# Performance work log

Hardware: AMD Instinct MI355X
Metric: run time of the kernel (lower is better)

The kernel has to match this reference:

```python
import jax, jax.numpy as jnp
import numpy as np

HEADS = 4
ATTN_DIM = 32
SCALE = ATTN_DIM ** -0.5
EPS = 1e-12  # F.normalize eps


def rmsnorm_chan(x, g):
    # x: (b, c, h, w); RMSNorm over channel dim: F.normalize(x, dim=1) * g * sqrt(c)
    c = x.shape[1]
    n = jnp.sqrt(jnp.sum(x * x, axis=1, keepdims=True))
    return x / jnp.maximum(n, EPS) * g[None, :, None, None] * jnp.sqrt(jnp.asarray(c, x.dtype))


def setup_inputs() -> dict:
    key = jax.random.key(0)
    ks = jax.random.split(key, 4)
    b, c, h, w = 16, 256, 64, 64
    hidden = HEADS * ATTN_DIM  # 128
    x = jax.random.normal(ks[0], (b, c, h, w), dtype=jnp.float32)
    norm_g = jnp.ones((c,), jnp.float32)
    w_qkv = jax.random.normal(ks[1], (3 * hidden, c), dtype=jnp.float32) * 0.02
    mem_kv = jax.random.normal(ks[2], (2, HEADS, ATTN_DIM, 4), dtype=jnp.float32)
    w_out = jax.random.normal(ks[3], (c, hidden), dtype=jnp.float32) * 0.02
    b_out = jnp.zeros((c,), jnp.float32)
    out_norm_g = jnp.ones((c,), jnp.float32)
    return {"x": x, "norm_g": norm_g, "w_qkv": w_qkv, "mem_kv": mem_kv,
            "w_out": w_out, "b_out": b_out, "out_norm_g": out_norm_g}


def reference(x, norm_g, w_qkv, mem_kv, w_out, b_out, out_norm_g):
    b, c, h, w = x.shape
    n = h * w
    xn = rmsnorm_chan(x, norm_g).reshape(b, c, n)  # pre-norm, flatten spatial
    # 1x1 conv (no bias) == channel matmul: (b, 3*hidden, n)
    qkv = jnp.einsum('oc,bcn->bon', w_qkv, xn)
    q, k, v = jnp.split(qkv, 3, axis=1)
    # (b, heads, d, n)
    q = q.reshape(b, HEADS, ATTN_DIM, n)
    k = k.reshape(b, HEADS, ATTN_DIM, n)
    v = v.reshape(b, HEADS, ATTN_DIM, n)
    # prepend memory kv (broadcast over batch): (b, heads, d, num_mem + n)
    mk = jnp.broadcast_to(mem_kv[0][None], (b, HEADS, ATTN_DIM, mem_kv.shape[-1]))
    mv = jnp.broadcast_to(mem_kv[1][None], (b, HEADS, ATTN_DIM, mem_kv.shape[-1]))
    k = jnp.concatenate([mk, k], axis=-1)
    v = jnp.concatenate([mv, v], axis=-1)
    q = jax.nn.softmax(q, axis=-2) * SCALE  # softmax over feature dim d
    k = jax.nn.softmax(k, axis=-1)          # softmax over token dim n
    context = jnp.einsum('bhdn,bhen->bhde', k, v)   # small d x e per head
    out = jnp.einsum('bhde,bhdn->bhen', context, q)  # (b, heads, e, n)
    out = out.reshape(b, HEADS * ATTN_DIM, h, w)
    # 1x1 conv with bias, then RMSNorm
    out = jnp.einsum('oc,bchw->bohw', w_out, out) + b_out[None, :, None, None]
    return rmsnorm_chan(out, out_norm_g)
```

## Files before the change

kernel.cpp:

```cpp
#include <hip/hip_runtime.h>
#include <hip/hip_bf16.h>

typedef __hip_bfloat16 bf16;
typedef __attribute__((ext_vector_type(8))) short bf16x8;
typedef __attribute__((ext_vector_type(4))) float floatx4;

#define NB 16
#define NC 256
#define NPIX 4096
#define NHID 128
#define NH 4
#define ND 32
#define NMEM 4
#define QSCALE 0.17677669529663687f

__launch_bounds__(256)
__global__ void kW(const float* __restrict__ wqkv, const float* __restrict__ g,
                   bf16* __restrict__ wgpack, float* __restrict__ zbase){
  const int u = blockIdx.x*256 + threadIdx.x;
  for (int z = u; z < 65536 + 2048; z += 48*256) zbase[z] = 0.f;
  const int s = u / 1536;
  const int r = u - s*1536;
  const int tile = r >> 6, l = r & 63;
  const int row = tile*16 + (l & 15);
  const int kb  = s*32 + (l >> 4)*8;
  const float* wp = wqkv + (size_t)row*NC + kb;
  floatx4 w0 = *(const floatx4*)wp;
  floatx4 w1 = *(const floatx4*)(wp + 4);
  floatx4 g0 = *(const floatx4*)(g + kb);
  floatx4 g1 = *(const floatx4*)(g + kb + 4);
  alignas(16) bf16 tmp[8];
  #pragma unroll
  for (int i = 0; i < 4; ++i){
    tmp[i]   = __float2bfloat16(w0[i]*g0[i]);
    tmp[4+i] = __float2bfloat16(w1[i]*g1[i]);
  }
  *(uint4*)(wgpack + (size_t)u*8) = *(const uint4*)tmp;
}

__launch_bounds__(256)
__global__ void kA(const float* __restrict__ x, const bf16* __restrict__ wgpack,
                   float* __restrict__ dout,
                   float* __restrict__ ctxu, float* __restrict__ zacc){
  __shared__ char smem alignas(16) [21632];
  bf16 (*Pb)[40] = (bf16(*)[40])smem;
  bf16 (*Vb)[40] = (bf16(*)[40])(smem + 10240);
  float* ssqL = (float*)(smem + 20480);
  float* sL   = (float*)(smem + 21504);
  const int t = threadIdx.x;
  const int bx = blockIdx.x, b = blockIdx.y;
  const int pb32 = bx * 32;
  const int pb64 = (bx >> 1) * 64, hi = bx & 1;
  const int wv = t >> 6, lane = t & 63, m = lane & 15, q4 = lane >> 4;
  const int px_st = t & 31, cg_st = t >> 5;
  const float* xb = x + (size_t)b*NC*NPIX;
  float ssq = 0.f;
  float xr[2][4];
  bf16x8 af[2][6];

  auto xissue = [&](int c, float* dst){
    const float* xp = xb + (size_t)(c*32 + cg_st*4)*NPIX + pb32 + px_st;
    #pragma unroll
    for (int j = 0; j < 4; ++j) dst[j] = xp[(size_t)j*NPIX];
  };
  auto xwrite = [&](int c, const float* v){
    alignas(8) bf16 tmp[4];
    #pragma unroll
    for (int j = 0; j < 4; ++j){
      ssq += v[j]*v[j];
      tmp[j] = __float2bfloat16(v[j]);
    }
    bf16 (*Xb)[40] = (bf16(*)[40])(smem + (c&1)*2560);
    *(uint2*)&Xb[px_st][cg_st*4] = *(const uint2*)tmp;
  };
  auto wload = [&](int c, int rt)->bf16x8 {
    return *(const bf16x8*)(wgpack + ((size_t)(c*24 + wv*6 + rt)*64 + lane)*8);
  };

  xissue(0, xr[0]);
  #pragma unroll
  for (int rt = 0; rt < 6; ++rt) af[0][rt] = wload(0, rt);
  xissue(1, xr[1]);
  xwrite(0, xr[0]);
  __syncthreads();

  floatx4 acc[6][2] = {};
  #pragma unroll
  for (int s = 0; s < 8; ++s){
    const int buf = s & 1;
    bf16 (*Xb)[40] = (bf16(*)[40])(smem + buf*2560);
    bf16x8 bfr[2];
    #pragma unroll
    for (int pt = 0; pt < 2; ++pt)
      bfr[pt] = *(const bf16x8*)&Xb[pt*16 + m][q4*8];
    if (s < 7){
      #pragma unroll
      for (int rt = 0; rt < 6; ++rt) af[(s+1)&1][rt] = wload(s + 1, rt);
    }
    if (s < 6) xissue(s + 2, xr[buf]);
    #pragma unroll
    for (int rt = 0; rt < 6; ++rt)
      #pragma unroll
      for (int pt = 0; pt < 2; ++pt)
        acc[rt][pt] = __builtin_amdgcn_mfma_f32_16x16x32_bf16(af[buf][rt], bfr[pt], acc[rt][pt], 0, 0, 0);
    if (s < 7) xwrite(s + 1, xr[buf ^ 1]);
    __syncthreads();
  }
  ssqL[cg_st*32 + px_st] = ssq;
  __syncthreads();
  if (t < 32){
    float tot = 0.f;
    #pragma unroll
    for (int i = 0; i < 8; ++i) tot += ssqL[i*32 + t];
    sL[t] = 16.0f / fmaxf(sqrtf(tot), 1e-12f);
  }
  __syncthreads();
  float sv[2];
  #pragma unroll
  for (int pt = 0; pt < 2; ++pt) sv[pt] = sL[pt*16 + m];
  #pragma unroll
  for (int pr = 0; pr < 3; ++pr){
    const int ra = 2*pr, rb = 2*pr + 1;
    const int row0 = wv*96 + pr*32;
    const int type = row0 >> 7;
    if (type == 0){
      const int slice = row0 >> 5;
      const int j0 = (q4 & 1)*4;
      #pragma unroll
      for (int pt = 0; pt < 2; ++pt){
        float va[4], vb[4];
        float mx = -1e30f;
        #pragma unroll
        for (int r = 0; r < 4; ++r){
          va[r] = acc[ra][pt][r]*sv[pt];
          vb[r] = acc[rb][pt][r]*sv[pt];
          mx = fmaxf(mx, fmaxf(va[r], vb[r]));
        }
        mx = fmaxf(mx, __shfl_xor(mx, 16, 64));
        mx = fmaxf(mx, __shfl_xor(mx, 32, 64));
        float se = 0.f;
        #pragma unroll
        for (int r = 0; r < 4; ++r){
          va[r] = __expf(va[r] - mx); vb[r] = __expf(vb[r] - mx);
          se += va[r] + vb[r];
        }
        se += __shfl_xor(se, 16, 64);
        se += __shfl_xor(se, 32, 64);
        const float inv = QSCALE / se;
        alignas(8) bf16 pka[4], pkb[4];
        #pragma unroll
        for (int r = 0; r < 4; ++r){
          pka[r] = __float2bfloat16(va[r]*inv);
          pkb[r] = __float2bfloat16(vb[r]*inv);
        }
        const int ca = (slice*4 + (hi*2 + pt))*4 + (q4 >> 1);
        const int cb = ca + 2;
        bf16* pa = (bf16*)(dout + (size_t)(b*NC + ca)*NPIX + pb64) + m*8 + j0;
        bf16* pv = (bf16*)(dout + (size_t)(b*NC + cb)*NPIX + pb64) + m*8 + j0;
        *(uint2*)pa = *(const uint2*)pka;
        *(uint2*)pv = *(const uint2*)pkb;
      }
    } else if (type == 1){
      const int d0 = row0 - 128;
      float za[4] = {}, zb[4] = {};
      #pragma unroll
      for (int pt = 0; pt < 2; ++pt){
        #pragma unroll
        for (int r = 0; r < 4; ++r){
          float pa = __expf(acc[ra][pt][r]*sv[pt]);
          float pv = __expf(acc[rb][pt][r]*sv[pt]);
          za[r] += pa; zb[r] += pv;
          Pb[d0      + q4*4 + r][pt*16 + m] = __float2bfloat16(pa);
          Pb[d0 + 16 + q4*4 + r][pt*16 + m] = __float2bfloat16(pv);
        }
      }
      #pragma unroll
      for (int r = 0; r < 4; ++r){
        #pragma unroll
        for (int o = 1; o < 16; o <<= 1){
          za[r] += __shfl_xor(za[r], o, 64);
          zb[r] += __shfl_xor(zb[r], o, 64);
        }
      }
      if (m == 0){
        #pragma unroll
        for (int r = 0; r < 4; ++r){
          atomicAdd(&zacc[b*NHID + d0      + q4*4 + r], za[r]);
          atomicAdd(&zacc[b*NHID + d0 + 16 + q4*4 + r], zb[r]);
        }
      }
    } else {
      const int v0 = row0 - 256;
      #pragma unroll
      for (int pt = 0; pt < 2; ++pt)
        #pragma unroll
        for (int r = 0; r < 4; ++r){
          Vb[v0      + q4*4 + r][pt*16 + m] = __float2bfloat16(acc[ra][pt][r]*sv[pt]);
          Vb[v0 + 16 + q4*4 + r][pt*16 + m] = __float2bfloat16(acc[rb][pt][r]*sv[pt]);
        }
    }
  }
  __syncthreads();
  floatx4 cx[2][2] = {};
  {
    bf16x8 af2[2], bf2[2];
    #pragma unroll
    for (int dt = 0; dt < 2; ++dt) af2[dt] = *(const bf16x8*)&Pb[wv*32 + dt*16 + m][q4*8];
    #pragma unroll
    for (int et = 0; et < 2; ++et) bf2[et] = *(const bf16x8*)&Vb[wv*32 + et*16 + m][q4*8];
    #pragma unroll
    for (int dt = 0; dt < 2; ++dt)
      #pragma unroll
      for (int et = 0; et < 2; ++et)
        cx[dt][et] = __builtin_amdgcn_mfma_f32_16x16x32_bf16(af2[dt], bf2[et], cx[dt][et], 0, 0, 0);
  }
  float* cb2 = ctxu + (size_t)(b*NH + wv)*ND*ND;
  #pragma unroll
  for (int dt = 0; dt < 2; ++dt)
    #pragma unroll
    for (int et = 0; et < 2; ++et)
      #pragma unroll
      for (int r = 0; r < 4; ++r)
        atomicAdd(&cb2[(dt*16 + q4*4 + r)*ND + et*16 + m], cx[dt][et][r]);
}

__launch_bounds__(256)
__global__ void k4_weff(const float* __restrict__ ctxu, const float* __restrict__ zacc,
                        const float* __restrict__ memkv, const float* __restrict__ wout,
                        bf16* __restrict__ wpack){
  __shared__ float ctxL[4][32][32];
  __shared__ float woutL[64][129];
  const int t = threadIdx.x;
  const int o0 = blockIdx.x * 64, b = blockIdx.y;
  {
    const float* ws = wout + (size_t)o0*NHID;
    #pragma unroll
    for (int i = 0; i < 32; ++i){
      const int idx = i*256 + t;
      woutL[idx >> 7][idx & 127] = ws[idx];
    }
  }
  if (t < 128){
    const int h = t >> 5;
    const float* mk = memkv + t*NMEM;
    float me[4]; float z = zacc[b*NHID + t];
    #pragma unroll
    for (int j = 0; j < 4; ++j){ me[j] = __expf(mk[j]); z += me[j]; }
    const float invz = 1.0f / z;
    const float* cp = ctxu + (size_t)(b*NH*ND + t)*ND;
    const float* mv = memkv + (size_t)(NHID + h*ND)*NMEM;
    #pragma unroll
    for (int e = 0; e < ND; ++e){
      float ce = cp[e];
      #pragma unroll
      for (int j = 0; j < 4; ++j) ce += me[j]*mv[e*NMEM + j];
      ctxL[h][t & 31][e] = ce * invz;
    }
  }
  __syncthreads();
  const int ol = t & 63, g = t >> 6;
  float out[32] = {};
  #pragma unroll
  for (int e = 0; e < 32; ++e){
    const float we = woutL[ol][g*32 + e];
    #pragma unroll
    for (int d = 0; d < 32; ++d) out[d] += ctxL[g][d][e] * we;
  }
  const int o = o0 + ol, tile = o >> 4, m16 = o & 15;
  #pragma unroll
  for (int q4k = 0; q4k < 4; ++q4k){
    alignas(16) bf16 tmp[8];
    #pragma unroll
    for (int j = 0; j < 8; ++j) tmp[j] = __float2bfloat16(out[q4k*8 + j]);
    *(uint4*)(wpack + ((size_t)((b*4 + g)*16 + tile)*64 + q4k*16 + m16)*8) = *(const uint4*)tmp;
  }
}

__launch_bounds__(256)
__global__ void k5_out(float* dout, const bf16* __restrict__ wpack,
                       const float* __restrict__ bout, const float* __restrict__ gout){
  __shared__ float red[256];
  __shared__ float nf[64];
  const int t = threadIdx.x;
  const int pb = blockIdx.x * 64, b = blockIdx.y;
  const int wv = t >> 6, lane = t & 63, m = lane & 15, q4 = lane >> 4;
  bf16x8 wf[2][4], qf[2][4];
  auto loadw = [&](int s, bf16x8* dst){
    #pragma unroll
    for (int rt = 0; rt < 4; ++rt)
      dst[rt] = *(const bf16x8*)(wpack + ((size_t)((b*4 + s)*16 + wv*4 + rt)*64 + lane)*8);
  };
  auto loadq = [&](int s, bf16x8* dst){
    #pragma unroll
    for (int pt = 0; pt < 4; ++pt)
      dst[pt] = *(const bf16x8*)((const char*)(dout + (size_t)(b*NC + (s*4 + pt)*4 + q4)*NPIX + pb) + m*16);
  };
  loadw(0, wf[0]); loadq(0, qf[0]);
  loadw(1, wf[1]); loadq(1, qf[1]);
  floatx4 acc[4][4] = {};
  #pragma unroll
  for (int s = 0; s < 4; ++s){
    const int buf = s & 1;
    #pragma unroll
    for (int rt = 0; rt < 4; ++rt)
      #pragma unroll
      for (int pt = 0; pt < 4; ++pt)
        acc[rt][pt] = __builtin_amdgcn_mfma_f32_16x16x32_bf16(wf[buf][rt], qf[buf][pt], acc[rt][pt], 0, 0, 0);
    if (s < 2){ loadw(s + 2, wf[buf]); loadq(s + 2, qf[buf]); }
  }
  float ps[4] = {0.f, 0.f, 0.f, 0.f};
  #pragma unroll
  for (int rt = 0; rt < 4; ++rt){
    const int row = wv*64 + rt*16 + q4*4;
    #pragma unroll
    for (int r = 0; r < 4; ++r){
      const float bias = bout[row + r];
      #pragma unroll
      for (int pt = 0; pt < 4; ++pt){
        acc[rt][pt][r] += bias;
        ps[pt] += acc[rt][pt][r]*acc[rt][pt][r];
      }
    }
  }
  #pragma unroll
  for (int pt = 0; pt < 4; ++pt){
    ps[pt] += __shfl_xor(ps[pt], 16, 64);
    ps[pt] += __shfl_xor(ps[pt], 32, 64);
  }
  if (q4 == 0){
    #pragma unroll
    for (int pt = 0; pt < 4; ++pt) red[wv*64 + pt*16 + m] = ps[pt];
  }
  __syncthreads();
  if (t < 64){
    float tot = red[t] + red[64 + t] + red[128 + t] + red[192 + t];
    nf[t] = 16.0f / fmaxf(sqrtf(tot), 1e-12f);
  }
  __syncthreads();
  float nv[4];
  #pragma unroll
  for (int pt = 0; pt < 4; ++pt) nv[pt] = nf[pt*16 + m];
  #pragma unroll
  for (int rt = 0; rt < 4; ++rt){
    const int row = wv*64 + rt*16 + q4*4;
    #pragma unroll
    for (int r = 0; r < 4; ++r){
      const float gg = gout[row + r];
      float* op = dout + (size_t)(b*NC + row + r)*NPIX + pb + m;
      #pragma unroll
      for (int pt = 0; pt < 4; ++pt)
        op[pt*16] = acc[rt][pt][r]*nv[pt]*gg;
    }
  }
}

extern "C" void kernel_launch(void* const* d_in, const int* in_sizes, int n_in,
                              void* d_out, int out_size, void* d_ws, size_t ws_size,
                              hipStream_t stream) {
  (void)in_sizes; (void)n_in; (void)out_size; (void)ws_size;
  const float* x     = (const float*)d_in[0];
  const float* ng    = (const float*)d_in[1];
  const float* wqkv  = (const float*)d_in[2];
  const float* memkv = (const float*)d_in[3];
  const float* wout  = (const float*)d_in[4];
  const float* bout  = (const float*)d_in[5];
  const float* gout  = (const float*)d_in[6];
  float* dout = (float*)d_out;
  char* ws = (char*)d_ws;
  bf16*  wgpack = (bf16*)(ws);
  bf16*  wpack  = (bf16*)(ws + 196608);
  float* ctxu   = (float*)(ws + 1245184);
  float* zacc   = (float*)(ws + 1507328);

  kW     <<<dim3(48),      256, 0, stream>>>(wqkv, ng, wgpack, ctxu);
  kA     <<<dim3(128, 16), 256, 0, stream>>>(x, wgpack, dout, ctxu, zacc);
  k4_weff<<<dim3(4, 16),   256, 0, stream>>>(ctxu, zacc, memkv, wout, wpack);
  k5_out <<<dim3(64, 16),  256, 0, stream>>>(dout, wpack, bout, gout);
}
```

Measured before the change: 199.1 us.

## Widen kA to 64-pixel tiles with 512 threads and register-direct x loads

kA now runs 512-thread blocks, each covering 64 pixels. Waves split into four row groups and two pixel halves. Each lane loads x straight from global memory into MFMA B fragments, so the LDS staging, double buffering and per-step barriers are gone. The channel sum of squares is now reduced with wave shuffles. The two pixel halves combine their context partials through LDS before one atomic per element, which halves the global atomics. In exchange the global loads are strided per lane with no prefetch pipelining, and the larger block may hurt occupancy.

```diff
diff --git a/kernel.cpp b/kernel.cpp
--- a/kernel.cpp
+++ b/kernel.cpp
@@ -38,111 +38,91 @@
   *(uint4*)(wgpack + (size_t)u*8) = *(const uint4*)tmp;
 }
 
-__launch_bounds__(256)
+__launch_bounds__(512, 4)
 __global__ void kA(const float* __restrict__ x, const bf16* __restrict__ wgpack,
                    float* __restrict__ dout,
                    float* __restrict__ ctxu, float* __restrict__ zacc){
-  __shared__ char smem alignas(16) [21632];
-  bf16 (*Pb)[40] = (bf16(*)[40])smem;
-  bf16 (*Vb)[40] = (bf16(*)[40])(smem + 10240);
-  float* ssqL = (float*)(smem + 20480);
-  float* sL   = (float*)(smem + 21504);
+  __shared__ char smem alignas(16) [36864];
+  bf16 (*Pb)[72] = (bf16(*)[72])smem;
+  bf16 (*Vb)[72] = (bf16(*)[72])(smem + 18432);
+  float* cxL = (float*)smem;
   const int t = threadIdx.x;
-  const int bx = blockIdx.x, b = blockIdx.y;
-  const int pb32 = bx * 32;
-  const int pb64 = (bx >> 1) * 64, hi = bx & 1;
+  const int pb = blockIdx.x * 64, b = blockIdx.y;
   const int wv = t >> 6, lane = t & 63, m = lane & 15, q4 = lane >> 4;
-  const int px_st = t & 31, cg_st = t >> 5;
-  const float* xb = x + (size_t)b*NC*NPIX;
-  float ssq = 0.f;
-  float xr[2][4];
-  bf16x8 af[2][6];
-
-  auto xissue = [&](int c, float* dst){
-    const float* xp = xb + (size_t)(c*32 + cg_st*4)*NPIX + pb32 + px_st;
-    #pragma unroll
-    for (int j = 0; j < 4; ++j) dst[j] = xp[(size_t)j*NPIX];
-  };
-  auto xwrite = [&](int c, const float* v){
-    alignas(8) bf16 tmp[4];
-    #pragma unroll
-    for (int j = 0; j < 4; ++j){
-      ssq += v[j]*v[j];
-      tmp[j] = __float2bfloat16(v[j]);
-    }
-    bf16 (*Xb)[40] = (bf16(*)[40])(smem + (c&1)*2560);
-    *(uint2*)&Xb[px_st][cg_st*4] = *(const uint2*)tmp;
-  };
-  auto wload = [&](int c, int rt)->bf16x8 {
-    return *(const bf16x8*)(wgpack + ((size_t)(c*24 + wv*6 + rt)*64 + lane)*8);
-  };
-
-  xissue(0, xr[0]);
-  #pragma unroll
-  for (int rt = 0; rt < 6; ++rt) af[0][rt] = wload(0, rt);
-  xissue(1, xr[1]);
-  xwrite(0, xr[0]);
-  __syncthreads();
-
+  const int rg = wv & 3, ph = wv >> 2;
+  const float* xb = x + (size_t)b*NC*NPIX + pb;
+
+  float ssqv[2] = {0.f, 0.f};
   floatx4 acc[6][2] = {};
+  bf16x8 af[6];
+  #pragma unroll
+  for (int rt = 0; rt < 6; ++rt)
+    af[rt] = *(const bf16x8*)(wgpack + ((size_t)(rg*6 + rt)*64 + lane)*8);
   #pragma unroll
   for (int s = 0; s < 8; ++s){
-    const int buf = s & 1;
-    bf16 (*Xb)[40] = (bf16(*)[40])(smem + buf*2560);
+    float xf[2][8];
+    #pragma unroll
+    for (int pt = 0; pt < 2; ++pt){
+      const float* xp = xb + (size_t)(s*32 + q4*8)*NPIX + (ph*2 + pt)*16 + m;
+      #pragma unroll
+      for (int j = 0; j < 8; ++j) xf[pt][j] = xp[(size_t)j*NPIX];
+    }
     bf16x8 bfr[2];
     #pragma unroll
-    for (int pt = 0; pt < 2; ++pt)
-      bfr[pt] = *(const bf16x8*)&Xb[pt*16 + m][q4*8];
+    for (int pt = 0; pt < 2; ++pt){
+      alignas(16) bf16 tmp[8];
+      #pragma unroll
+      for (int j = 0; j < 8; ++j){
+        ssqv[pt] += xf[pt][j]*xf[pt][j];
+        tmp[j] = __float2bfloat16(xf[pt][j]);
+      }
+      bfr[pt] = *(const bf16x8*)tmp;
+    }
+    #pragma unroll
+    for (int rt = 0; rt < 6; ++rt)
+      #pragma unroll
+      for (int pt = 0; pt < 2; ++pt)
+        acc[rt][pt] = __builtin_amdgcn_mfma_f32_16x16x32_bf16(af[rt], bfr[pt], acc[rt][pt], 0, 0, 0);
     if (s < 7){
       #pragma unroll
-      for (int rt = 0; rt < 6; ++rt) af[(s+1)&1][rt] = wload(s + 1, rt);
-    }
-    if (s < 6) xissue(s + 2, xr[buf]);
-    #pragma unroll
-    for (int rt = 0; rt < 6; ++rt)
-      #pragma unroll
-      for (int pt = 0; pt < 2; ++pt)
-        acc[rt][pt] = __builtin_amdgcn_mfma_f32_16x16x32_bf16(af[buf][rt], bfr[pt], acc[rt][pt], 0, 0, 0);
-    if (s < 7) xwrite(s + 1, xr[buf ^ 1]);
-    __syncthreads();
-  }
-  ssqL[cg_st*32 + px_st] = ssq;
-  __syncthreads();
-  if (t < 32){
-    float tot = 0.f;
-    #pragma unroll
-    for (int i = 0; i < 8; ++i) tot += ssqL[i*32 + t];
-    sL[t] = 16.0f / fmaxf(sqrtf(tot), 1e-12f);
-  }
-  __syncthreads();
+      for (int rt = 0; rt < 6; ++rt)
+        af[rt] = *(const bf16x8*)(wgpack + ((size_t)((s+1)*24 + rg*6 + rt)*64 + lane)*8);
+    }
+  }
   float sv[2];
   #pragma unroll
-  for (int pt = 0; pt < 2; ++pt) sv[pt] = sL[pt*16 + m];
+  for (int pt = 0; pt < 2; ++pt){
+    float tot = ssqv[pt];
+    tot += __shfl_xor(tot, 16, 64);
+    tot += __shfl_xor(tot, 32, 64);
+    sv[pt] = 16.0f / fmaxf(sqrtf(tot), 1e-12f);
+  }
   #pragma unroll
   for (int pr = 0; pr < 3; ++pr){
     const int ra = 2*pr, rb = 2*pr + 1;
-    const int row0 = wv*96 + pr*32;
+    const int row0 = rg*96 + pr*32;
     const int type = row0 >> 7;
     if (type == 0){
       const int slice = row0 >> 5;
       const int j0 = (q4 & 1)*4;
       #pragma unroll
       for (int pt = 0; pt < 2; ++pt){
-        float va[4], vb[4];
+        const int gpt = ph*2 + pt;
+        float va[4], vb4[4];
         float mx = -1e30f;
         #pragma unroll
         for (int r = 0; r < 4; ++r){
-          va[r] = acc[ra][pt][r]*sv[pt];
-          vb[r] = acc[rb][pt][r]*sv[pt];
-          mx = fmaxf(mx, fmaxf(va[r], vb[r]));
+          va[r]  = acc[ra][pt][r]*sv[pt];
+          vb4[r] = acc[rb][pt][r]*sv[pt];
+          mx = fmaxf(mx, fmaxf(va[r], vb4[r]));
         }
         mx = fmaxf(mx, __shfl_xor(mx, 16, 64));
         mx = fmaxf(mx, __shfl_xor(mx, 32, 64));
         float se = 0.f;
         #pragma unroll
         for (int r = 0; r < 4; ++r){
-          va[r] = __expf(va[r] - mx); vb[r] = __expf(vb[r] - mx);
-          se += va[r] + vb[r];
+          va[r] = __expf(va[r] - mx); vb4[r] = __expf(vb4[r] - mx);
+          se += va[r] + vb4[r];
         }
         se += __shfl_xor(se, 16, 64);
         se += __shfl_xor(se, 32, 64);
@@ -151,12 +131,12 @@
         #pragma unroll
         for (int r = 0; r < 4; ++r){
           pka[r] = __float2bfloat16(va[r]*inv);
-          pkb[r] = __float2bfloat16(vb[r]*inv);
-        }
-        const int ca = (slice*4 + (hi*2 + pt))*4 + (q4 >> 1);
+          pkb[r] = __float2bfloat16(vb4[r]*inv);
+        }
+        const int ca = (slice*4 + gpt)*4 + (q4 >> 1);
         const int cb = ca + 2;
-        bf16* pa = (bf16*)(dout + (size_t)(b*NC + ca)*NPIX + pb64) + m*8 + j0;
-        bf16* pv = (bf16*)(dout + (size_t)(b*NC + cb)*NPIX + pb64) + m*8 + j0;
+        bf16* pa = (bf16*)(dout + (size_t)(b*NC + ca)*NPIX + pb) + m*8 + j0;
+        bf16* pv = (bf16*)(dout + (size_t)(b*NC + cb)*NPIX + pb) + m*8 + j0;
         *(uint2*)pa = *(const uint2*)pka;
         *(uint2*)pv = *(const uint2*)pkb;
       }
@@ -165,13 +145,14 @@
       float za[4] = {}, zb[4] = {};
       #pragma unroll
       for (int pt = 0; pt < 2; ++pt){
+        const int gpt = ph*2 + pt;
         #pragma unroll
         for (int r = 0; r < 4; ++r){
           float pa = __expf(acc[ra][pt][r]*sv[pt]);
           float pv = __expf(acc[rb][pt][r]*sv[pt]);
           za[r] += pa; zb[r] += pv;
-          Pb[d0      + q4*4 + r][pt*16 + m] = __float2bfloat16(pa);
-          Pb[d0 + 16 + q4*4 + r][pt*16 + m] = __float2bfloat16(pv);
+          Pb[d0      + q4*4 + r][gpt*16 + m] = __float2bfloat16(pa);
+          Pb[d0 + 16 + q4*4 + r][gpt*16 + m] = __float2bfloat16(pv);
         }
       }
       #pragma unroll
@@ -192,36 +173,53 @@
     } else {
       const int v0 = row0 - 256;
       #pragma unroll
-      for (int pt = 0; pt < 2; ++pt)
-        #pragma unroll
-        for (int r = 0; r < 4; ++r){
-          Vb[v0      + q4*4 + r][pt*16 + m] = __float2bfloat16(acc[ra][pt][r]*sv[pt]);
-          Vb[v0 + 16 + q4*4 + r][pt*16 + m] = __float2bfloat16(acc[rb][pt][r]*sv[pt]);
-        }
+      for (int pt = 0; pt < 2; ++pt){
+        const int gpt = ph*2 + pt;
+        #pragma unroll
+        for (int r = 0; r < 4; ++r){
+          Vb[v0      + q4*4 + r][gpt*16 + m] = __float2bfloat16(acc[ra][pt][r]*sv[pt]);
+          Vb[v0 + 16 + q4*4 + r][gpt*16 + m] = __float2bfloat16(acc[rb][pt][r]*sv[pt]);
+        }
+      }
     }
   }
   __syncthreads();
   floatx4 cx[2][2] = {};
   {
-    bf16x8 af2[2], bf2[2];
-    #pragma unroll
-    for (int dt = 0; dt < 2; ++dt) af2[dt] = *(const bf16x8*)&Pb[wv*32 + dt*16 + m][q4*8];
-    #pragma unroll
-    for (int et = 0; et < 2; ++et) bf2[et] = *(const bf16x8*)&Vb[wv*32 + et*16 + m][q4*8];
+    const int k0t = ph*32;
+    bf16x8 paf[2], pvf[2];
+    #pragma unroll
+    for (int dt = 0; dt < 2; ++dt) paf[dt] = *(const bf16x8*)&Pb[rg*32 + dt*16 + m][k0t + q4*8];
+    #pragma unroll
+    for (int et = 0; et < 2; ++et) pvf[et] = *(const bf16x8*)&Vb[rg*32 + et*16 + m][k0t + q4*8];
     #pragma unroll
     for (int dt = 0; dt < 2; ++dt)
       #pragma unroll
       for (int et = 0; et < 2; ++et)
-        cx[dt][et] = __builtin_amdgcn_mfma_f32_16x16x32_bf16(af2[dt], bf2[et], cx[dt][et], 0, 0, 0);
-  }
-  float* cb2 = ctxu + (size_t)(b*NH + wv)*ND*ND;
-  #pragma unroll
-  for (int dt = 0; dt < 2; ++dt)
-    #pragma unroll
-    for (int et = 0; et < 2; ++et)
-      #pragma unroll
-      for (int r = 0; r < 4; ++r)
-        atomicAdd(&cb2[(dt*16 + q4*4 + r)*ND + et*16 + m], cx[dt][et][r]);
+        cx[dt][et] = __builtin_amdgcn_mfma_f32_16x16x32_bf16(paf[dt], pvf[et], cx[dt][et], 0, 0, 0);
+  }
+  __syncthreads();
+  if (ph == 1){
+    #pragma unroll
+    for (int dt = 0; dt < 2; ++dt)
+      #pragma unroll
+      for (int et = 0; et < 2; ++et)
+        #pragma unroll
+        for (int r = 0; r < 4; ++r)
+          cxL[rg*1024 + (dt*16 + q4*4 + r)*32 + et*16 + m] = cx[dt][et][r];
+  }
+  __syncthreads();
+  if (ph == 0){
+    float* cb2 = ctxu + (size_t)(b*NH + rg)*ND*ND;
+    #pragma unroll
+    for (int dt = 0; dt < 2; ++dt)
+      #pragma unroll
+      for (int et = 0; et < 2; ++et)
+        #pragma unroll
+        for (int r = 0; r < 4; ++r)
+          atomicAdd(&cb2[(dt*16 + q4*4 + r)*ND + et*16 + m],
+                    cx[dt][et][r] + cxL[rg*1024 + (dt*16 + q4*4 + r)*32 + et*16 + m]);
+  }
 }
 
 __launch_bounds__(256)
@@ -373,7 +371,7 @@
   float* zacc   = (float*)(ws + 1507328);
 
   kW     <<<dim3(48),      256, 0, stream>>>(wqkv, ng, wgpack, ctxu);
-  kA     <<<dim3(128, 16), 256, 0, stream>>>(x, wgpack, dout, ctxu, zacc);
+  kA     <<<dim3(64, 16),  512, 0, stream>>>(x, wgpack, dout, ctxu, zacc);
   k4_weff<<<dim3(4, 16),   256, 0, stream>>>(ctxu, zacc, memkv, wout, wpack);
   k5_out <<<dim3(64, 16),  256, 0, stream>>>(dout, wpack, bout, gout);
 }
```

After: 199.1 us. About the same (-0.0%).
